# Kernel tuning notes

Hardware: AMD Instinct MI355X
Metric: run time of the kernel (lower is better)

The kernel has to match this reference:

```python
import jax, jax.numpy as jnp
import numpy as np

Bb, H, L = 4, 512, 4096      # batch, d_model, seq len
N2 = 32                       # d_state//2 complex conjugate-pair modes
Cch = 1                       # channels
DM = 512                      # d_model (output dim)

def setup_inputs() -> dict:
    key = jax.random.key(0)
    ks = jax.random.split(key, 8)
    u = jax.random.normal(ks[0], (Bb, H, L), jnp.float32)
    # dt ~ LogUniform[1e-3, 1e-1] as in S4 defaults
    log_dt = (jax.random.uniform(ks[1], (H,), jnp.float32)
              * (np.log(0.1) - np.log(0.001)) + np.log(0.001)).astype(jnp.float32)
    # S4D-Lin initialization: A = -1/2 + i*pi*n
    A_re = -0.5 * jnp.ones((H, N2), jnp.float32)
    A_im = jnp.broadcast_to(np.pi * jnp.arange(N2, dtype=np.float32), (H, N2)).astype(jnp.float32)
    B_re = jnp.ones((H, N2), jnp.float32)
    B_im = jnp.zeros((H, N2), jnp.float32)
    C_re = jax.random.normal(ks[2], (Cch, H, N2), jnp.float32) * (N2 ** -0.5)
    C_im = jax.random.normal(ks[3], (Cch, H, N2), jnp.float32) * (N2 ** -0.5)
    D = jax.random.normal(ks[4], (Cch, H), jnp.float32)
    W_out = jax.random.normal(ks[5], (2 * DM, Cch * H), jnp.float32) * ((Cch * H) ** -0.5)
    b_out = jnp.zeros((2 * DM,), jnp.float32)
    return {"u": u, "log_dt": log_dt, "A_re": A_re, "A_im": A_im,
            "B_re": B_re, "B_im": B_im, "C_re": C_re, "C_im": C_im,
            "D": D, "W_out": W_out, "b_out": b_out}

def reference(u, log_dt, A_re, A_im, B_re, B_im, C_re, C_im, D, W_out, b_out):
    # --- SSM kernel generation (diag / S4D, ZOH discretization) ---
    dt = jnp.exp(log_dt)                      # (H,)
    A = A_re + 1j * A_im                      # (H, N2)
    Bc = B_re + 1j * B_im                     # (H, N2)
    Cc = C_re + 1j * C_im                     # (C, H, N2)
    dtA = dt[:, None] * A                     # (H, N2)
    dB = (jnp.exp(dtA) - 1.0) / A * Bc        # (H, N2)
    pos = jnp.arange(L, dtype=jnp.float32)
    V = jnp.exp(dtA[:, :, None] * pos)        # (H, N2, L) Vandermonde of dA^l
    # factor 2 accounts for conjugate-pair halves
    k = (2.0 * jnp.einsum('chn,hn,hnl->chl', Cc, dB, V).real).astype(u.dtype)  # (C,H,L)
    # --- FFT convolution: y = k * u (causal, linear conv via zero-padded FFT) ---
    n_fft = 2 * L
    k_f = jnp.fft.rfft(k, n=n_fft)            # (C, H, L+1)
    u_f = jnp.fft.rfft(u, n=n_fft)            # (B, H, L+1)
    y_f = jnp.einsum('bhl,chl->bchl', u_f, k_f)
    y = jnp.fft.irfft(y_f, n=n_fft)[..., :L]  # (B, C, H, L)
    # skip connection D
    y = y + jnp.einsum('bhl,ch->bchl', u, D)
    y = y.reshape(u.shape[0], Cch * H, L)     # 'b c h l -> b (c h) l'
    # pointwise activation (exact GELU, matching torch default)
    y = jax.nn.gelu(y, approximate=False)
    # output linear (transposed, kernel-size-1) + GLU over channel dim
    z = jnp.einsum('bhl,oh->bol', y, W_out) + b_out[None, :, None]  # (B, 2*DM, L)
    out = z[:, :DM] * jax.nn.sigmoid(z[:, DM:])                      # (B, DM, L)
    return out
```

## Files before the change

kernel.cpp:

```cpp
#include <hip/hip_runtime.h>
#include <math.h>

#define BB 4
#define HH 512
#define LL 4096
#define NN 32
#define DMOUT 512

typedef __attribute__((ext_vector_type(8))) short short8;
typedef __attribute__((ext_vector_type(4))) float f32x4;

__device__ __forceinline__ unsigned f2bf(float x) {
    unsigned u = __float_as_uint(x);
    return (u + 0x7fffu + ((u >> 16) & 1u)) >> 16;
}
__device__ __forceinline__ unsigned packhl(float x) {
    unsigned hb = f2bf(x);
    float xh = __uint_as_float(hb << 16);
    return (hb << 16) | f2bf(x - xh);
}
__device__ __forceinline__ float reconhl(unsigned v) {
    return __uint_as_float(v & 0xffff0000u) + __uint_as_float(v << 16);
}
__device__ __forceinline__ void gload_lds16(const void* g, void* l) {
    __builtin_amdgcn_global_load_lds((const __attribute__((address_space(1))) void*)g,
                                     (__attribute__((address_space(3))) void*)l, 16, 0, 0);
}

__global__ __launch_bounds__(256) void prep_kernel(
    const float* __restrict__ log_dt,
    const float* __restrict__ A_re, const float* __restrict__ A_im,
    const float* __restrict__ B_re, const float* __restrict__ B_im,
    const float* __restrict__ C_re, const float* __restrict__ C_im,
    const float* __restrict__ W,
    unsigned* __restrict__ A3t, unsigned* __restrict__ Et,
    unsigned short* __restrict__ whi, int preW) {
    const int h = blockIdx.x;
    const int tid = threadIdx.x;
    __shared__ float cst_lds[256];

    if (preW) {
        int i = (h * 256 + tid) * 4;
        float4 wv = *(const float4*)(W + i);
        ushort4 o;
        o.x = (unsigned short)f2bf(wv.x);
        o.y = (unsigned short)f2bf(wv.y);
        o.z = (unsigned short)f2bf(wv.z);
        o.w = (unsigned short)f2bf(wv.w);
        *(ushort4*)(whi + i) = o;
    }

    if (tid < 32) {
        int n = tid;
        float dt = expf(log_dt[h]);
        float ar = A_re[h * NN + n], ai = A_im[h * NN + n];
        float dtar = dt * ar, dtai = dt * ai;
        float ea = expf(dtar);
        float s, c; sincosf(dtai, &s, &c);
        float dA_r = ea * c, dA_i = ea * s;
        float em_r = dA_r - 1.0f, em_i = dA_i;
        float inv = 1.0f / (ar * ar + ai * ai);
        float t_r = (em_r * ar + em_i * ai) * inv;
        float t_i = (em_i * ar - em_r * ai) * inv;
        float br = B_re[h * NN + n], bi = B_im[h * NN + n];
        cst_lds[0 * 32 + n] = dtar;
        cst_lds[1 * 32 + n] = dtai;
        cst_lds[2 * 32 + n] = dA_r;
        cst_lds[3 * 32 + n] = dA_i;
        cst_lds[4 * 32 + n] = t_r * br - t_i * bi;
        cst_lds[5 * 32 + n] = t_r * bi + t_i * br;
        cst_lds[6 * 32 + n] = 2.0f * C_re[h * NN + n];
        cst_lds[7 * 32 + n] = 2.0f * C_im[h * NN + n];
    }
    __syncthreads();

    const int n = tid & 31, q = tid >> 5;
    const float dtar = cst_lds[0 * 32 + n], dtai = cst_lds[1 * 32 + n];
    const float dAr = cst_lds[2 * 32 + n], dAi = cst_lds[3 * 32 + n];
    const float dbr = cst_lds[4 * 32 + n], dbi = cst_lds[5 * 32 + n];
    const float tcr = cst_lds[6 * 32 + n], tci = cst_lds[7 * 32 + n];

    {
        float p = (float)(56 - q * 8);
        float mr = expf(p * dtar);
        float s, c; sincosf(p * dtai, &s, &c);
        float pr = mr * c, pi = mr * s;
        unsigned* base = A3t + (size_t)h * 4096;
#pragma unroll
        for (int jj = 7; jj >= 0; jj--) {
            int m = q * 8 + jj;
            base[m * 64 + n]      = packhl(dbr * pr - dbi * pi);
            base[m * 64 + 32 + n] = packhl(dbr * pi + dbi * pr);
            float nr2 = pr * dAr - pi * dAi;
            pi = pr * dAi + pi * dAr;
            pr = nr2;
        }
    }
    {
        float p = (float)(q * 8 + 1);
        float mr = expf(p * dtar);
        float s, c; sincosf(p * dtai, &s, &c);
        float pr = mr * c, pi = mr * s;
        unsigned* base = Et + (size_t)h * 4096;
#pragma unroll
        for (int i = q * 8; i <= q * 8 + 7; i++) {
            base[i * 64 + n]      = packhl(tcr * pr - tci * pi);
            base[i * 64 + 32 + n] = packhl(-(tcr * pi + tci * pr));
            float nr2 = pr * dAr - pi * dAi;
            pi = pr * dAi + pi * dAr;
            pr = nr2;
        }
    }
}

__global__ __launch_bounds__(256, 4) void ssm_kernel(
    const float* __restrict__ u, const float* __restrict__ log_dt,
    const float* __restrict__ A_re, const float* __restrict__ A_im,
    const float* __restrict__ B_re, const float* __restrict__ B_im,
    const float* __restrict__ C_re, const float* __restrict__ C_im,
    const float* __restrict__ D,
    const unsigned* __restrict__ A3t, const unsigned* __restrict__ Et,
    unsigned short* __restrict__ yhi) {
    const int h = blockIdx.x;
    const int b = blockIdx.y;
    const int tid = threadIdx.x;
    const int lane = tid & 63;
    const int w = tid >> 6;
    const int g = lane >> 4;
    const int l15 = lane & 15;

    __shared__ unsigned short uh[64 * 72];
    __shared__ unsigned short ul[64 * 72];
    __shared__ unsigned XsR[32 * 65];
    __shared__ unsigned XsI[32 * 65];
    __shared__ unsigned karr_pk[128];
    __shared__ float kpart[256];
    __shared__ float cst_lds[256];

    {
        const float* urow = u + ((size_t)(b * HH + h)) * LL;
#pragma unroll
        for (int r = 0; r < 4; r++) {
            int f = tid + 256 * r;
            float4 v = *(const float4*)(urow + f * 4);
            int t = f >> 4, mb = (f & 15) << 2;
            unsigned hx = f2bf(v.x), hy = f2bf(v.y), hz = f2bf(v.z), hw = f2bf(v.w);
            uint2 hwv;
            hwv.x = hx | (hy << 16);
            hwv.y = hz | (hw << 16);
            float rx = v.x - __uint_as_float(hx << 16);
            float ry = v.y - __uint_as_float(hy << 16);
            float rz = v.z - __uint_as_float(hz << 16);
            float rw = v.w - __uint_as_float(hw << 16);
            uint2 lwv;
            lwv.x = f2bf(rx) | (f2bf(ry) << 16);
            lwv.y = f2bf(rz) | (f2bf(rw) << 16);
            *(uint2*)(&uh[t * 72 + mb]) = hwv;
            *(uint2*)(&ul[t * 72 + mb]) = lwv;
        }
    }
    if (tid < 32) {
        int n = tid;
        float dt = expf(log_dt[h]);
        float ar = A_re[h * NN + n], ai = A_im[h * NN + n];
        float dtar = dt * ar, dtai = dt * ai;
        float ea = expf(dtar);
        float s, c; sincosf(dtai, &s, &c);
        float dA_r = ea * c, dA_i = ea * s;
        float em_r = dA_r - 1.0f, em_i = dA_i;
        float inv = 1.0f / (ar * ar + ai * ai);
        float t_r = (em_r * ar + em_i * ai) * inv;
        float t_i = (em_i * ar - em_r * ai) * inv;
        float br = B_re[h * NN + n], bi = B_im[h * NN + n];
        cst_lds[0 * 32 + n] = dtar;
        cst_lds[1 * 32 + n] = dtai;
        cst_lds[2 * 32 + n] = dA_r;
        cst_lds[3 * 32 + n] = dA_i;
        cst_lds[4 * 32 + n] = t_r * br - t_i * bi;
        cst_lds[5 * 32 + n] = t_r * bi + t_i * br;
        cst_lds[6 * 32 + n] = 2.0f * C_re[h * NN + n];
        cst_lds[7 * 32 + n] = 2.0f * C_im[h * NN + n];
    }
    __syncthreads();

    {
        int nprime = w * 16 + l15;
        const unsigned* a3b = A3t + (size_t)h * 4096 + nprime;
        short8 a3h0, a3l0, a3h1, a3l1;
#pragma unroll
        for (int j = 0; j < 8; j++) {
            unsigned v = a3b[(g * 8 + j) * 64];
            a3h0[j] = (short)(v >> 16); a3l0[j] = (short)(v & 0xffffu);
            unsigned v2 = a3b[(32 + g * 8 + j) * 64];
            a3h1[j] = (short)(v2 >> 16); a3l1[j] = (short)(v2 & 0xffffu);
        }
#pragma unroll
        for (int ni = 0; ni < 4; ni++) {
            int t = ni * 16 + l15;
            short8 uH0 = *(const short8*)(uh + t * 72 + g * 8);
            short8 uL0 = *(const short8*)(ul + t * 72 + g * 8);
            short8 uH1 = *(const short8*)(uh + t * 72 + 32 + g * 8);
            short8 uL1 = *(const short8*)(ul + t * 72 + 32 + g * 8);
            f32x4 a = (f32x4){0.f, 0.f, 0.f, 0.f};
            a = __builtin_amdgcn_mfma_f32_16x16x32_bf16(a3h0, uH0, a, 0, 0, 0);
            a = __builtin_amdgcn_mfma_f32_16x16x32_bf16(a3l0, uH0, a, 0, 0, 0);
            a = __builtin_amdgcn_mfma_f32_16x16x32_bf16(a3h0, uL0, a, 0, 0, 0);
            a = __builtin_amdgcn_mfma_f32_16x16x32_bf16(a3h1, uH1, a, 0, 0, 0);
            a = __builtin_amdgcn_mfma_f32_16x16x32_bf16(a3l1, uH1, a, 0, 0, 0);
            a = __builtin_amdgcn_mfma_f32_16x16x32_bf16(a3h1, uL1, a, 0, 0, 0);
            int nprime2 = w * 16 + g * 4;
#pragma unroll
            for (int r = 0; r < 4; r++) {
                int nn2 = nprime2 + r;
                if (nn2 < 32) XsR[nn2 * 65 + t] = __float_as_uint(a[r]);
                else          XsI[(nn2 - 32) * 65 + t] = __float_as_uint(a[r]);
            }
        }
    }
    {
        int j = tid & 63, nr = tid >> 6;
        float acc = 0.0f;
        if (j == 0) {
#pragma unroll
            for (int q = 0; q < 8; q++) {
                int n = nr * 8 + q;
                acc = fmaf(cst_lds[6 * 32 + n], cst_lds[4 * 32 + n], acc);
                acc = fmaf(-cst_lds[7 * 32 + n], cst_lds[5 * 32 + n], acc);
            }
        } else {
            const unsigned* eb = Et + (size_t)h * 4096 + (j - 1) * 64;
#pragma unroll
            for (int q = 0; q < 8; q++) {
                int n = nr * 8 + q;
                acc = fmaf(reconhl(eb[n]), cst_lds[4 * 32 + n], acc);
                acc = fmaf(reconhl(eb[32 + n]), cst_lds[5 * 32 + n], acc);
            }
        }
        kpart[nr * 64 + j] = acc;
    }
    short8 e0h, e0l, e1h, e1l;
    {
        int i = w * 16 + l15;
        const unsigned* eb = Et + (size_t)h * 4096 + i * 64;
#pragma unroll
        for (int j = 0; j < 8; j++) {
            int n = g * 8 + j;
            unsigned v = eb[n];
            e0h[j] = (short)(v >> 16); e0l[j] = (short)(v & 0xffffu);
            unsigned v2 = eb[32 + n];
            e1h[j] = (short)(v2 >> 16); e1l[j] = (short)(v2 & 0xffffu);
        }
    }
    __syncthreads();

    if (tid < 32) {
        int n = tid;
        float dtar = cst_lds[0 * 32 + n], dtai = cst_lds[1 * 32 + n];
        float mr = expf(64.0f * dtar);
        float s, c; sincosf(64.0f * dtai, &s, &c);
        float Mr = mr * c, Mi = mr * s;
        float cr = 0.f, ci = 0.f;
        unsigned* pR = XsR + n * 65;
        unsigned* pI = XsI + n * 65;
        float fr = __uint_as_float(pR[0]);
        float fi2 = __uint_as_float(pI[0]);
#pragma unroll 4
        for (int t = 0; t < 64; t++) {
            float frn = 0.f, fin = 0.f;
            if (t < 63) { frn = __uint_as_float(pR[t + 1]); fin = __uint_as_float(pI[t + 1]); }
            pR[t] = packhl(cr);
            pI[t] = packhl(ci);
            float nr = fmaf(Mr, cr, fmaf(-Mi, ci, fr));
            float nic = fmaf(Mr, ci, fmaf(Mi, cr, fi2));
            cr = nr; ci = nic;
            fr = frn; fi2 = fin;
        }
    } else if (tid >= 64 && tid < 128) {
        int j = tid - 64;
        float k = kpart[j] + kpart[64 + j] + kpart[128 + j] + kpart[192 + j];
        karr_pk[64 + j] = packhl(k);
    } else if (tid >= 128 && tid < 192) {
        karr_pk[tid - 128] = 0u;
    }
    __syncthreads();

    {
        int i = w * 16 + l15;
        short8 kh0, kl0, kh1, kl1;
#pragma unroll
        for (int j = 0; j < 8; j++) {
            unsigned v0 = karr_pk[64 + i - (g * 8 + j)];
            kh0[j] = (short)(v0 >> 16); kl0[j] = (short)(v0 & 0xffffu);
            unsigned v1 = karr_pk[64 + i - (32 + g * 8 + j)];
            kh1[j] = (short)(v1 >> 16); kl1[j] = (short)(v1 & 0xffffu);
        }
        float Dh = D[h];
        unsigned short* orow = yhi + ((size_t)(b * HH + h)) * LL;
#pragma unroll
        for (int ni = 0; ni < 4; ni++) {
            int t = ni * 16 + l15;
            short8 uH0 = *(const short8*)(uh + t * 72 + g * 8);
            short8 uL0 = *(const short8*)(ul + t * 72 + g * 8);
            short8 uH1 = *(const short8*)(uh + t * 72 + 32 + g * 8);
            short8 uL1 = *(const short8*)(ul + t * 72 + 32 + g * 8);
            short8 xrh, xrl, xih, xil;
#pragma unroll
            for (int j = 0; j < 8; j++) {
                unsigned v = XsR[(g * 8 + j) * 65 + t];
                xrh[j] = (short)(v >> 16); xrl[j] = (short)(v & 0xffffu);
                unsigned v2 = XsI[(g * 8 + j) * 65 + t];
                xih[j] = (short)(v2 >> 16); xil[j] = (short)(v2 & 0xffffu);
            }
            f32x4 a = (f32x4){0.f, 0.f, 0.f, 0.f};
            a = __builtin_amdgcn_mfma_f32_16x16x32_bf16(kh0, uH0, a, 0, 0, 0);
            a = __builtin_amdgcn_mfma_f32_16x16x32_bf16(kl0, uH0, a, 0, 0, 0);
            a = __builtin_amdgcn_mfma_f32_16x16x32_bf16(kh0, uL0, a, 0, 0, 0);
            a = __builtin_amdgcn_mfma_f32_16x16x32_bf16(kh1, uH1, a, 0, 0, 0);
            a = __builtin_amdgcn_mfma_f32_16x16x32_bf16(kl1, uH1, a, 0, 0, 0);
            a = __builtin_amdgcn_mfma_f32_16x16x32_bf16(kh1, uL1, a, 0, 0, 0);
            a = __builtin_amdgcn_mfma_f32_16x16x32_bf16(e0h, xrh, a, 0, 0, 0);
            a = __builtin_amdgcn_mfma_f32_16x16x32_bf16(e0h, xrl, a, 0, 0, 0);
            a = __builtin_amdgcn_mfma_f32_16x16x32_bf16(e0l, xrh, a, 0, 0, 0);
            a = __builtin_amdgcn_mfma_f32_16x16x32_bf16(e1h, xih, a, 0, 0, 0);
            a = __builtin_amdgcn_mfma_f32_16x16x32_bf16(e1h, xil, a, 0, 0, 0);
            a = __builtin_amdgcn_mfma_f32_16x16x32_bf16(e1l, xih, a, 0, 0, 0);
            ushort4 ov;
            unsigned short* op = &ov.x;
#pragma unroll
            for (int r = 0; r < 4; r++) {
                int io = w * 16 + g * 4 + r;
                float uv = __uint_as_float(((unsigned)uh[t * 72 + io]) << 16)
                         + __uint_as_float(((unsigned)ul[t * 72 + io]) << 16);
                float y = a[r] + Dh * uv;
                float gl = 0.5f * y * (1.0f + erff(y * 0.70710678118654752f));
                op[r] = (unsigned short)f2bf(gl);
            }
            *(ushort4*)(&orow[t * 64 + w * 16 + g * 4]) = ov;
        }
    }
}

__global__ __launch_bounds__(256) void gemm_glu_mfma(const unsigned short* __restrict__ yhi,
                                                     const float* __restrict__ W,
                                                     const unsigned short* __restrict__ whi,
                                                     const float* __restrict__ bias,
                                                     float* __restrict__ out, int preW) {
    const int b = blockIdx.z;
    const int d0 = blockIdx.y * 64;
    const int l0 = blockIdx.x * 64;
    const int tid = threadIdx.x;
    const int lane = tid & 63;
    const int wid = tid >> 6;
    const int wave_m = wid & 1;
    const int wave_n = wid >> 1;
    const int l15 = lane & 15;
    const int g = lane >> 4;

    __shared__ unsigned short Ysh[2][32 * 64];
    __shared__ char Wlds[2][128 * 64];

    f32x4 acc[4][2];
#pragma unroll
    for (int i = 0; i < 4; i++)
#pragma unroll
        for (int j = 0; j < 2; j++) acc[i][j] = (f32x4){0.f, 0.f, 0.f, 0.f};

#define STAGE(BUF, KT)                                                                   \
    {                                                                                    \
        const int h0s = (KT) * 32;                                                       \
        {                                                                                \
            int kr = tid >> 3;                                                           \
            int cc = tid & 7;                                                            \
            int scol = (cc * 8) ^ ((kr & 8) ? 8 : 0);                                    \
            const unsigned short* srcY = yhi + ((size_t)(b * HH + h0s + kr)) * LL + l0 + scol; \
            gload_lds16(srcY, (char*)Ysh[BUF] + tid * 16);                               \
        }                                                                                \
        if (preW) {                                                                      \
            _Pragma("unroll")                                                            \
            for (int e = 0; e < 2; e++) {                                                \
                int c = e * 256 + tid;                                                   \
                int row = c >> 2;                                                        \
                int gx = c & 3;                                                          \
                int qq = (row >> 1) & 3;                                                 \
                int grow = (row < 64) ? (d0 + row) : (448 + d0 + row);                   \
                const unsigned short* srcW = whi + (size_t)grow * 512 + h0s + ((gx ^ qq) * 8); \
                gload_lds16(srcW, Wlds[BUF] + c * 16);                                   \
            }                                                                            \
        } else {                                                                         \
            int row = tid >> 1;                                                          \
            int kb = (tid & 1) * 16;                                                     \
            int qq = (row >> 1) & 3;                                                     \
            int grow = (row < 64) ? (d0 + row) : (448 + d0 + row);                       \
            const float* srcW = W + (size_t)grow * 512 + h0s + kb;                       \
            float4 w0 = *(const float4*)(srcW);                                          \
            float4 w1 = *(const float4*)(srcW + 4);                                      \
            float4 w2 = *(const float4*)(srcW + 8);                                      \
            float4 w3 = *(const float4*)(srcW + 12);                                     \
            short8 v0, v1;                                                               \
            v0[0] = (short)f2bf(w0.x); v0[1] = (short)f2bf(w0.y);                        \
            v0[2] = (short)f2bf(w0.z); v0[3] = (short)f2bf(w0.w);                        \
            v0[4] = (short)f2bf(w1.x); v0[5] = (short)f2bf(w1.y);                        \
            v0[6] = (short)f2bf(w1.z); v0[7] = (short)f2bf(w1.w);                        \
            v1[0] = (short)f2bf(w2.x); v1[1] = (short)f2bf(w2.y);                        \
            v1[2] = (short)f2bf(w2.z); v1[3] = (short)f2bf(w2.w);                        \
            v1[4] = (short)f2bf(w3.x); v1[5] = (short)f2bf(w3.y);                        \
            v1[6] = (short)f2bf(w3.z); v1[7] = (short)f2bf(w3.w);                        \
            int g0 = kb >> 3;                                                            \
            *(short8*)(Wlds[BUF] + row * 64 + ((g0 ^ qq) * 16)) = v0;                    \
            *(short8*)(Wlds[BUF] + row * 64 + (((g0 + 1) ^ qq) * 16)) = v1;              \
        }                                                                                \
    }

    STAGE(0, 0)
    __syncthreads();

    int cur = 0;
    for (int kt = 0; kt < 16; kt++) {
        if (kt < 15) STAGE(cur ^ 1, kt + 1)

        short8 af[4];
#pragma unroll
        for (int mi = 0; mi < 4; mi++) {
            int rowb = (mi < 2) ? (wave_m * 32 + mi * 16) : (64 + wave_m * 32 + (mi - 2) * 16);
            int row = rowb + l15;
            int qq = (row >> 1) & 3;
            af[mi] = *(const short8*)(Wlds[cur] + row * 64 + ((g ^ qq) * 16));
        }
#pragma unroll
        for (int ni = 0; ni < 2; ni++) {
            int col = wave_n * 32 + ni * 16 + l15;
            int cs = col ^ ((g & 1) << 3);
            const unsigned short* yb = Ysh[cur] + (8 * g) * 64 + cs;
            short8 bh;
            bh[0] = (short)yb[0 * 64];
            bh[1] = (short)yb[1 * 64];
            bh[2] = (short)yb[2 * 64];
            bh[3] = (short)yb[3 * 64];
            bh[4] = (short)yb[4 * 64];
            bh[5] = (short)yb[5 * 64];
            bh[6] = (short)yb[6 * 64];
            bh[7] = (short)yb[7 * 64];
#pragma unroll
            for (int mi = 0; mi < 4; mi++) {
                acc[mi][ni] = __builtin_amdgcn_mfma_f32_16x16x32_bf16(af[mi], bh, acc[mi][ni], 0, 0, 0);
            }
        }
        __syncthreads();
        cur ^= 1;
    }
#undef STAGE

#pragma unroll
    for (int mi = 0; mi < 2; mi++) {
        int dbase = d0 + wave_m * 32 + mi * 16 + (g << 2);
#pragma unroll
        for (int r = 0; r < 4; r++) {
            int d = dbase + r;
            float b1 = bias[d], b2 = bias[DMOUT + d];
#pragma unroll
            for (int ni = 0; ni < 2; ni++) {
                int l = l0 + wave_n * 32 + ni * 16 + l15;
                float z1 = acc[mi][ni][r] + b1;
                float z2 = acc[mi + 2][ni][r] + b2;
                out[((size_t)(b * DMOUT + d)) * LL + l] = z1 * (1.0f / (1.0f + expf(-z2)));
            }
        }
    }
}

extern "C" void kernel_launch(void* const* d_in, const int* in_sizes, int n_in,
                              void* d_out, int out_size, void* d_ws, size_t ws_size,
                              hipStream_t stream) {
    const float* u      = (const float*)d_in[0];
    const float* log_dt = (const float*)d_in[1];
    const float* A_re   = (const float*)d_in[2];
    const float* A_im   = (const float*)d_in[3];
    const float* B_re   = (const float*)d_in[4];
    const float* B_im   = (const float*)d_in[5];
    const float* C_re   = (const float*)d_in[6];
    const float* C_im   = (const float*)d_in[7];
    const float* D      = (const float*)d_in[8];
    const float* W      = (const float*)d_in[9];
    const float* bias   = (const float*)d_in[10];
    float* out = (float*)d_out;

    char* ws = (char*)d_ws;
    unsigned short* yhi = (unsigned short*)ws;
    unsigned* A3t = (unsigned*)(ws + 16777216);
    unsigned* Et  = (unsigned*)(ws + 16777216 + 8388608);
    unsigned short* whi = (unsigned short*)(ws + 33554432);
    int preW = (ws_size >= (size_t)(33554432 + 1048576)) ? 1 : 0;

    prep_kernel<<<HH, 256, 0, stream>>>(log_dt, A_re, A_im, B_re, B_im, C_re, C_im,
                                        W, A3t, Et, whi, preW);
    ssm_kernel<<<dim3(HH, BB), 256, 0, stream>>>(u, log_dt, A_re, A_im, B_re, B_im,
                                                 C_re, C_im, D, A3t, Et, yhi);
    gemm_glu_mfma<<<dim3(64, 8, BB), 256, 0, stream>>>(yhi, W, whi, bias, out, preW);
}
```

Measured before the change: 88.53 us.

## Transpose scan LDS buffers for vector access and use fast GELU/sigmoid

Changes the XsR/XsI shared buffers from mode-major (stride 65) to time-major (stride 36) layout. This lets MFMA results be stored as uint4 and operand fragments loaded with 16-byte LDS reads instead of scalar gathers. Replaces the exact erf-based GELU with the tanh-form approximation computed through a fast exp sigmoid, and uses __expf in the GLU sigmoid. The new stride may add bank conflicts in the serial recurrence, and the GELU approximation introduces a small numerical deviation from exact GELU.

```diff
diff --git a/kernel.cpp b/kernel.cpp
--- a/kernel.cpp
+++ b/kernel.cpp
@@ -21,6 +21,10 @@
 }
 __device__ __forceinline__ float reconhl(unsigned v) {
     return __uint_as_float(v & 0xffff0000u) + __uint_as_float(v << 16);
+}
+__device__ __forceinline__ float gelu_fast(float y) {
+    float s2 = y * fmaf(y * y, 0.044715f, 1.0f) * 1.5957691216057308f;
+    return y * (1.0f / (1.0f + __expf(-s2)));
 }
 __device__ __forceinline__ void gload_lds16(const void* g, void* l) {
     __builtin_amdgcn_global_load_lds((const __attribute__((address_space(1))) void*)g,
@@ -131,8 +135,8 @@
 
     __shared__ unsigned short uh[64 * 72];
     __shared__ unsigned short ul[64 * 72];
-    __shared__ unsigned XsR[32 * 65];
-    __shared__ unsigned XsI[32 * 65];
+    __shared__ unsigned XsR[64 * 36];
+    __shared__ unsigned XsI[64 * 36];
     __shared__ unsigned karr_pk[128];
     __shared__ float kpart[256];
     __shared__ float cst_lds[256];
@@ -194,6 +198,7 @@
             unsigned v2 = a3b[(32 + g * 8 + j) * 64];
             a3h1[j] = (short)(v2 >> 16); a3l1[j] = (short)(v2 & 0xffffu);
         }
+        int nprime2 = w * 16 + g * 4;
 #pragma unroll
         for (int ni = 0; ni < 4; ni++) {
             int t = ni * 16 + l15;
@@ -208,13 +213,11 @@
             a = __builtin_amdgcn_mfma_f32_16x16x32_bf16(a3h1, uH1, a, 0, 0, 0);
             a = __builtin_amdgcn_mfma_f32_16x16x32_bf16(a3l1, uH1, a, 0, 0, 0);
             a = __builtin_amdgcn_mfma_f32_16x16x32_bf16(a3h1, uL1, a, 0, 0, 0);
-            int nprime2 = w * 16 + g * 4;
-#pragma unroll
-            for (int r = 0; r < 4; r++) {
-                int nn2 = nprime2 + r;
-                if (nn2 < 32) XsR[nn2 * 65 + t] = __float_as_uint(a[r]);
-                else          XsI[(nn2 - 32) * 65 + t] = __float_as_uint(a[r]);
-            }
+            uint4 wv;
+            wv.x = __float_as_uint(a[0]); wv.y = __float_as_uint(a[1]);
+            wv.z = __float_as_uint(a[2]); wv.w = __float_as_uint(a[3]);
+            if (nprime2 < 32) *(uint4*)(&XsR[t * 36 + nprime2]) = wv;
+            else              *(uint4*)(&XsI[t * 36 + (nprime2 - 32)]) = wv;
         }
     }
     {
@@ -260,16 +263,16 @@
         float s, c; sincosf(64.0f * dtai, &s, &c);
         float Mr = mr * c, Mi = mr * s;
         float cr = 0.f, ci = 0.f;
-        unsigned* pR = XsR + n * 65;
-        unsigned* pI = XsI + n * 65;
+        unsigned* pR = XsR + n;
+        unsigned* pI = XsI + n;
         float fr = __uint_as_float(pR[0]);
         float fi2 = __uint_as_float(pI[0]);
 #pragma unroll 4
         for (int t = 0; t < 64; t++) {
             float frn = 0.f, fin = 0.f;
-            if (t < 63) { frn = __uint_as_float(pR[t + 1]); fin = __uint_as_float(pI[t + 1]); }
-            pR[t] = packhl(cr);
-            pI[t] = packhl(ci);
+            if (t < 63) { frn = __uint_as_float(pR[(t + 1) * 36]); fin = __uint_as_float(pI[(t + 1) * 36]); }
+            pR[t * 36] = packhl(cr);
+            pI[t * 36] = packhl(ci);
             float nr = fmaf(Mr, cr, fmaf(-Mi, ci, fr));
             float nic = fmaf(Mr, ci, fmaf(Mi, cr, fi2));
             cr = nr; ci = nic;
@@ -303,14 +306,27 @@
             short8 uL0 = *(const short8*)(ul + t * 72 + g * 8);
             short8 uH1 = *(const short8*)(uh + t * 72 + 32 + g * 8);
             short8 uL1 = *(const short8*)(ul + t * 72 + 32 + g * 8);
+            uint4 r0 = *(const uint4*)(&XsR[t * 36 + g * 8]);
+            uint4 r1 = *(const uint4*)(&XsR[t * 36 + g * 8 + 4]);
+            uint4 i0 = *(const uint4*)(&XsI[t * 36 + g * 8]);
+            uint4 i1 = *(const uint4*)(&XsI[t * 36 + g * 8 + 4]);
             short8 xrh, xrl, xih, xil;
-#pragma unroll
-            for (int j = 0; j < 8; j++) {
-                unsigned v = XsR[(g * 8 + j) * 65 + t];
-                xrh[j] = (short)(v >> 16); xrl[j] = (short)(v & 0xffffu);
-                unsigned v2 = XsI[(g * 8 + j) * 65 + t];
-                xih[j] = (short)(v2 >> 16); xil[j] = (short)(v2 & 0xffffu);
-            }
+            xrh[0] = (short)(r0.x >> 16); xrl[0] = (short)(r0.x & 0xffffu);
+            xrh[1] = (short)(r0.y >> 16); xrl[1] = (short)(r0.y & 0xffffu);
+            xrh[2] = (short)(r0.z >> 16); xrl[2] = (short)(r0.z & 0xffffu);
+            xrh[3] = (short)(r0.w >> 16); xrl[3] = (short)(r0.w & 0xffffu);
+            xrh[4] = (short)(r1.x >> 16); xrl[4] = (short)(r1.x & 0xffffu);
+            xrh[5] = (short)(r1.y >> 16); xrl[5] = (short)(r1.y & 0xffffu);
+            xrh[6] = (short)(r1.z >> 16); xrl[6] = (short)(r1.z & 0xffffu);
+            xrh[7] = (short)(r1.w >> 16); xrl[7] = (short)(r1.w & 0xffffu);
+            xih[0] = (short)(i0.x >> 16); xil[0] = (short)(i0.x & 0xffffu);
+            xih[1] = (short)(i0.y >> 16); xil[1] = (short)(i0.y & 0xffffu);
+            xih[2] = (short)(i0.z >> 16); xil[2] = (short)(i0.z & 0xffffu);
+            xih[3] = (short)(i0.w >> 16); xil[3] = (short)(i0.w & 0xffffu);
+            xih[4] = (short)(i1.x >> 16); xil[4] = (short)(i1.x & 0xffffu);
+            xih[5] = (short)(i1.y >> 16); xil[5] = (short)(i1.y & 0xffffu);
+            xih[6] = (short)(i1.z >> 16); xil[6] = (short)(i1.z & 0xffffu);
+            xih[7] = (short)(i1.w >> 16); xil[7] = (short)(i1.w & 0xffffu);
             f32x4 a = (f32x4){0.f, 0.f, 0.f, 0.f};
             a = __builtin_amdgcn_mfma_f32_16x16x32_bf16(kh0, uH0, a, 0, 0, 0);
             a = __builtin_amdgcn_mfma_f32_16x16x32_bf16(kl0, uH0, a, 0, 0, 0);
@@ -332,8 +348,7 @@
                 float uv = __uint_as_float(((unsigned)uh[t * 72 + io]) << 16)
                          + __uint_as_float(((unsigned)ul[t * 72 + io]) << 16);
                 float y = a[r] + Dh * uv;
-                float gl = 0.5f * y * (1.0f + erff(y * 0.70710678118654752f));
-                op[r] = (unsigned short)f2bf(gl);
+                op[r] = (unsigned short)f2bf(gelu_fast(y));
             }
             *(ushort4*)(&orow[t * 64 + w * 16 + g * 4]) = ov;
         }
@@ -462,7 +477,7 @@
                 int l = l0 + wave_n * 32 + ni * 16 + l15;
                 float z1 = acc[mi][ni][r] + b1;
                 float z2 = acc[mi + 2][ni][r] + b2;
-                out[((size_t)(b * DMOUT + d)) * LL + l] = z1 * (1.0f / (1.0f + expf(-z2)));
+                out[((size_t)(b * DMOUT + d)) * LL + l] = z1 * (1.0f / (1.0f + __expf(-z2)));
             }
         }
     }
```

After: 77.63 us. 12.3% less time.
